# Optimization experiments

Hardware: AMD Instinct MI355X
Metric: run time of the kernel (lower is better)

## Reference

```python
import jax, jax.numpy as jnp
import numpy as np

D_MODEL, N_HEAD, D_HEAD = 192, 16, 6
INNER = N_HEAD * D_HEAD  # 96
LN_EPS = 1e-9
INF = 1e6


def _rel_pos_embeds(S):
    # Funnel get_position_embeds, relative_shift path, block 0
    half = D_MODEL // 2
    freq = jnp.arange(half, dtype=jnp.float32)
    inv_freq = 1.0 / (10000.0 ** (freq / half))
    rel_pos_id = jnp.arange(-2 * S, 2 * S, dtype=jnp.float32)  # [4S]
    sinusoid = rel_pos_id[:, None] * inv_freq[None, :]          # [4S, half]
    pos_embed = jnp.concatenate([jnp.sin(sinusoid), jnp.cos(sinusoid)], axis=-1)  # [4S, D]
    # block 0: relative_pos(pos, stride=1) = arange(S, -S, -1), offset by 2S
    idx = jnp.arange(S, -S, -1) + 2 * S  # [2S]
    return pos_embed[idx]  # [2S, D]


def _relative_shift_gather(pos_attn, context_len):
    # shift = 1 (q_len == context_len)
    B, n, S, M = pos_attn.shape  # M = 2*S
    pa = pos_attn.reshape(B, n, M, S)[:, :, 1:, :]
    pa = pa.reshape(B, n, S, M - 1)[..., :context_len]
    return pa


def setup_inputs() -> dict:
    key = jax.random.key(0)
    ks = jax.random.split(key, 12)
    B, S = 4, 1024
    s = 0.02
    return {
        "x": jax.random.normal(ks[0], (B, S, D_MODEL), dtype=jnp.float32),
        "mask0": jnp.ones((B, S), dtype=jnp.float32),
        "Wq": jax.random.normal(ks[1], (D_MODEL, INNER), dtype=jnp.float32) * s,
        "Wk": jax.random.normal(ks[2], (D_MODEL, INNER), dtype=jnp.float32) * s,
        "bk": jnp.zeros((INNER,), dtype=jnp.float32),
        "Wv": jax.random.normal(ks[3], (D_MODEL, INNER), dtype=jnp.float32) * s,
        "bv": jnp.zeros((INNER,), dtype=jnp.float32),
        "Wo": jax.random.normal(ks[4], (INNER, D_MODEL), dtype=jnp.float32) * s,
        "bo": jnp.zeros((D_MODEL,), dtype=jnp.float32),
        "r_w_bias": jax.random.normal(ks[5], (N_HEAD, D_HEAD), dtype=jnp.float32) * s,
        "r_r_bias": jax.random.normal(ks[6], (N_HEAD, D_HEAD), dtype=jnp.float32) * s,
        "r_kernel": jax.random.normal(ks[7], (D_MODEL, N_HEAD, D_HEAD), dtype=jnp.float32) * s,
        "gamma": jnp.ones((D_MODEL,), dtype=jnp.float32),
        "beta": jnp.zeros((D_MODEL,), dtype=jnp.float32),
    }


def reference(x, mask0, Wq, Wk, bk, Wv, bv, Wo, bo, r_w_bias, r_r_bias, r_kernel, gamma, beta):
    B, S, _ = x.shape
    scale = 1.0 / np.sqrt(D_HEAD).astype(np.float32)

    q = (x @ Wq).reshape(B, S, N_HEAD, D_HEAD) * scale       # q_head pre-scaled
    k = (x @ Wk + bk).reshape(B, S, N_HEAD, D_HEAD)
    v = (x @ Wv + bv).reshape(B, S, N_HEAD, D_HEAD)

    # content score
    content = jnp.einsum("bind,bjnd->bnij", q + r_w_bias * scale, k)

    # positional score with relative shift
    r = _rel_pos_embeds(S)                                    # [2S, D]
    r_head = jnp.einsum("td,dnh->tnh", r, r_kernel)           # [2S, n, h]
    pos_attn = jnp.einsum("binh,tnh->bnit", q + r_r_bias * scale, r_head)  # [B,n,S,2S]
    pos_attn = _relative_shift_gather(pos_attn, S)            # [B,n,S,S]

    attn_score = content + pos_attn  # token_type_attn = 0 (no token_type_ids)
    attn_score = attn_score - INF * (1.0 - mask0[:, None, None, :])
    attn_prob = jax.nn.softmax(attn_score, axis=-1)

    attn_vec = jnp.einsum("bnij,bjnd->bind", attn_prob, v)    # [B,S,n,h]
    attn_out = attn_vec.reshape(B, S, INNER) @ Wo + bo

    h = x + attn_out
    mu = jnp.mean(h, axis=-1, keepdims=True)
    var = jnp.mean(jnp.square(h - mu), axis=-1, keepdims=True)
    out = (h - mu) / jnp.sqrt(var + LN_EPS) * gamma + beta
    return out
```

## Files before the change

### kernel.cpp

```cpp
#include <hip/hip_runtime.h>
#include <hip/hip_bf16.h>
#include <math.h>

#define LOG2E 1.4426950408889634f
#define IS6   0.4082482904638630f

typedef _Float16 h2 __attribute__((ext_vector_type(2)));

#if defined(__has_builtin)
#if __has_builtin(__builtin_amdgcn_fdot2)
#define FDOT2(a,b,c) __builtin_amdgcn_fdot2((a),(b),(c),false)
#endif
#if __has_builtin(__builtin_amdgcn_exp2f)
#define EXP2(x) __builtin_amdgcn_exp2f(x)
#endif
#endif
#ifndef FDOT2
#define FDOT2(a,b,c) ((float)(a).x*(float)(b).x + (float)(a).y*(float)(b).y + (c))
#endif
#ifndef EXP2
#define EXP2(x) exp2f(x)
#endif

__device__ __forceinline__ unsigned packh2(float x, float y) {
    h2 v; v.x = (_Float16)x; v.y = (_Float16)y;
    return *(unsigned*)&v;
}
__device__ __forceinline__ h2 ash2(unsigned u) { return *(h2*)&u; }
__device__ __forceinline__ unsigned ah2(h2 v) { return *(unsigned*)&v; }

#if defined(__has_builtin)
#if __has_builtin(__builtin_amdgcn_cvt_pkrtz)
__device__ __forceinline__ h2 pk2(float a, float b) {
    auto r = __builtin_amdgcn_cvt_pkrtz(a, b);
    union { decltype(r) f; h2 h; } c; c.f = r; return c.h;
}
#define HAVE_PK2 1
#endif
#endif
#ifndef HAVE_PK2
__device__ __forceinline__ h2 pk2(float a, float b) {
    h2 v; v.x = (_Float16)a; v.y = (_Float16)b; return v;
}
#endif

__global__ __launch_bounds__(96)
void k_wpack(const float* __restrict__ Wq, const float* __restrict__ Wk,
             const float* __restrict__ Wv, unsigned* __restrict__ Whp) {
    int bid = blockIdx.x;
    int mat = bid / 96, dp = bid - mat * 96;
    const float* W = mat == 0 ? Wq : (mat == 1 ? Wk : Wv);
    int c = threadIdx.x;
    float w0 = W[(2 * dp) * 96 + c];
    float w1 = W[(2 * dp + 1) * 96 + c];
    Whp[(mat * 96 + c) * 96 + dp] = packh2(w0, w1);
}

__global__ __launch_bounds__(256)
void k_pre(const float* __restrict__ x, const unsigned* __restrict__ Whp,
           const float* __restrict__ bk, const float* __restrict__ bv,
           const float* __restrict__ rwb, const float* __restrict__ rrb,
           const float* __restrict__ rk,
           unsigned* __restrict__ QWt, unsigned* __restrict__ QRt,
           unsigned* __restrict__ Kpl, unsigned* __restrict__ Vpl,
           unsigned short* __restrict__ phiB) {
    __shared__ unsigned xs[64 * 97];
    __shared__ float rrowS[4 * 192];
    int tid = threadIdx.x;
    if (blockIdx.x < 1152) {
        int rt = blockIdx.x / 18, qb = blockIdx.x - rt * 18;
        int row0 = rt * 64;
        for (int idx = tid; idx < 6144; idx += 256) {
            int r = idx / 96, dpp = idx - r * 96;
            float2 xv = *(const float2*)&x[(size_t)(row0 + r) * 192 + dpp * 2];
            xs[r * 97 + dpp] = packh2(xv.x, xv.y);
        }
        __syncthreads();
        int quad = __builtin_amdgcn_readfirstlane(tid >> 6);
        int sl = tid & 63;
        int cq = qb * 4 + quad;
        int c0 = cq * 4;
        int mat = c0 / 96, col0 = c0 - mat * 96;
        const unsigned* wb0 = Whp + (mat * 96 + col0) * 96;
        const unsigned* wb1 = wb0 + 96;
        const unsigned* wb2 = wb0 + 192;
        const unsigned* wb3 = wb0 + 288;
        const unsigned* xr = xs + sl * 97;
        float a0 = 0.f, a1 = 0.f, a2 = 0.f, a3 = 0.f;
        #pragma unroll 8
        for (int dp = 0; dp < 96; ++dp) {
            h2 xp = ash2(xr[dp]);
            a0 = FDOT2(xp, ash2(wb0[dp]), a0);
            a1 = FDOT2(xp, ash2(wb1[dp]), a1);
            a2 = FDOT2(xp, ash2(wb2[dp]), a2);
            a3 = FDOT2(xp, ash2(wb3[dp]), a3);
        }
        float av[4] = {a0, a1, a2, a3};
        int row = row0 + sl, b = row >> 10, s = row & 1023;
        if (mat == 0) {
            #pragma unroll
            for (int pp = 0; pp < 2; ++pp) {
                int cA = col0 + 2 * pp;
                int pg = cA >> 1;
                int nn = pg / 3, hp = pg - nn * 3;
                int bnn = b * 16 + nn;
                unsigned qw = packh2((av[2*pp]   + rwb[cA])   * (IS6 * LOG2E),
                                     (av[2*pp+1] + rwb[cA+1]) * (IS6 * LOG2E));
                unsigned qr = packh2((av[2*pp]   + rrb[cA])   * (IS6 * LOG2E),
                                     (av[2*pp+1] + rrb[cA+1]) * (IS6 * LOG2E));
                size_t qo = ((size_t)(hp * 64 + bnn) << 10) + s;
                QWt[qo] = qw;
                QRt[qo] = qr;
            }
        } else if (mat == 1) {
            #pragma unroll
            for (int pp = 0; pp < 2; ++pp) {
                int cA = col0 + 2 * pp;
                int pg = cA >> 1;
                int nn = pg / 3, hp = pg - nn * 3;
                int bnn = b * 16 + nn;
                Kpl[((size_t)(hp * 64 + bnn) << 10) + s] =
                    packh2(av[2*pp] + bk[cA], av[2*pp+1] + bk[cA+1]);
            }
        } else {
            #pragma unroll
            for (int pp = 0; pp < 2; ++pp) {
                int cA = col0 + 2 * pp;
                int pg = cA >> 1;
                int nn = pg / 3, hp = pg - nn * 3;
                int bnn = b * 16 + nn;
                Vpl[((size_t)(hp * 64 + bnn) << 10) + s] =
                    packh2(av[2*pp] + bv[cA], av[2*pp+1] + bv[cA+1]);
            }
        }
    } else {
        int t0 = (blockIdx.x - 1152) * 4;
        for (int idx = tid; idx < 768; idx += 256) {
            int tl = idx / 192, d = idx - tl * 192;
            int dd = d < 96 ? d : d - 96;
            float w = exp2f(-(float)dd * 0.13841367062030676f);
            float ang = (float)(1024 - (t0 + tl)) * w;
            rrowS[idx] = (d < 96) ? __sinf(ang) : __cosf(ang);
        }
        __syncthreads();
        if (tid < 192) {
            int c = tid % 96, tg = tid / 96;
            float acc0 = 0.f, acc1 = 0.f;
            #pragma unroll 4
            for (int d = 0; d < 192; ++d) {
                float wv = rk[d * 96 + c];
                acc0 += rrowS[(tg * 2 + 0) * 192 + d] * wv;
                acc1 += rrowS[(tg * 2 + 1) * 192 + d] * wv;
            }
            int n = c / 6, h = c - n * 6;
            _Float16 v0 = (_Float16)acc0, v1 = (_Float16)acc1;
            phiB[(n * 2048 + t0 + tg * 2 + 0) * 8 + h] = *(unsigned short*)&v0;
            phiB[(n * 2048 + t0 + tg * 2 + 1) * 8 + h] = *(unsigned short*)&v1;
            if (tg == 0 && c < 32) {
                int nn = c >> 1, hh = 6 + (c & 1);
                #pragma unroll
                for (int k = 0; k < 4; ++k)
                    phiB[(nn * 2048 + t0 + k) * 8 + hh] = 0;
            }
        }
    }
}

#define SWZ(r) ((r) ^ (((r) >> 3) & 7))
__global__ __launch_bounds__(256, 6)
void k_attn(const unsigned* __restrict__ QWt, const unsigned* __restrict__ QRt,
            const unsigned* __restrict__ Kpl, const unsigned* __restrict__ Vpl,
            const float* __restrict__ mask0,
            const unsigned short* __restrict__ phiB,
            uint4* __restrict__ P) {
    __shared__ uint4 phiS[1088];
    __shared__ uint4 kS[64];
    __shared__ unsigned vS[192];
    int tid = threadIdx.x;
    int jc = blockIdx.x, n = blockIdx.y, b = blockIdx.z;
    int j0 = jc * 64;
    int bn = b * 16 + n;

    const uint4* phg = (const uint4*)phiB + (n * 2048 + j0 + 1);
    for (int r = tid; r < 1088; r += 256) phiS[SWZ(r)] = phg[r];
    if (tid < 64) {
        int j = j0 + tid;
        size_t base = ((size_t)bn << 10) + j;
        float mt = 1e6f * (mask0[b * 1024 + j] - 1.0f) * LOG2E;
        kS[tid] = make_uint4(Kpl[base], Kpl[base + 65536], Kpl[base + 131072],
                             __float_as_uint(mt));
    } else if (tid < 128) {
        int r = tid - 64;
        int j = j0 + r;
        size_t base = ((size_t)bn << 10) + j;
        vS[r * 3 + 0] = Vpl[base];
        vS[r * 3 + 1] = Vpl[base + 65536];
        vS[r * 3 + 2] = Vpl[base + 131072];
    }
    __syncthreads();

    int iA = tid * 4;
    h2 qw[4][3], qr[4][3];
    #pragma unroll
    for (int hp = 0; hp < 3; ++hp) {
        size_t off = (size_t)hp * 65536 + ((size_t)bn << 10) + iA;
        uint4 qa = *(const uint4*)&QWt[off];
        qw[0][hp] = ash2(qa.x); qw[1][hp] = ash2(qa.y);
        qw[2][hp] = ash2(qa.z); qw[3][hp] = ash2(qa.w);
        uint4 ra = *(const uint4*)&QRt[off];
        qr[0][hp] = ash2(ra.x); qr[1][hp] = ash2(ra.y);
        qr[2][hp] = ash2(ra.z); qr[3][hp] = ash2(ra.w);
    }

    float den[4] = {0.f, 0.f, 0.f, 0.f};
    h2 zero2; zero2.x = (_Float16)0.f; zero2.y = (_Float16)0.f;
    h2 ac0[4], ac1[4], ac2[4];
    #pragma unroll
    for (int q = 0; q < 4; ++q) { ac0[q] = zero2; ac1[q] = zero2; ac2[q] = zero2; }

    int Cb = 1023 - iA;
    uint4 ph[4];
    ph[3] = phiS[SWZ(Cb - 1)];
    ph[2] = phiS[SWZ(Cb - 2)];
    ph[1] = phiS[SWZ(Cb - 3)];
    uint4 nxt = phiS[SWZ(Cb)];

    #pragma unroll 4
    for (int jj = 0; jj < 64; ++jj) {
        uint4 K = kS[jj];
        unsigned Vx = vS[3 * jj], Vy = vS[3 * jj + 1], Vz = vS[3 * jj + 2];
        ph[jj & 3] = nxt;
        nxt = phiS[SWZ(Cb + jj + 1)];
        float mt = __uint_as_float(K.w);
        h2 v01 = ash2(Vx), v23 = ash2(Vy), v45 = ash2(Vz);
        #pragma unroll
        for (int q = 0; q < 4; ++q) {
            uint4 p = ph[(jj - q) & 3];
            float sc = FDOT2(ash2(K.x), qw[q][0],
                       FDOT2(ash2(K.y), qw[q][1],
                       FDOT2(ash2(K.z), qw[q][2], mt)));
            sc = FDOT2(ash2(p.x), qr[q][0],
                 FDOT2(ash2(p.y), qr[q][1],
                 FDOT2(ash2(p.z), qr[q][2], sc)));
            float e = EXP2(sc);
            den[q] += e;
            h2 e2 = pk2(e, e);
            ac0[q] += e2 * v01;
            ac1[q] += e2 * v23;
            ac2[q] += e2 * v45;
        }
    }
    size_t pb = ((size_t)(jc * 64 + bn)) << 10;
    #pragma unroll
    for (int q = 0; q < 4; ++q) {
        uint4 st;
        st.x = __float_as_uint(den[q]);
        st.y = ah2(ac0[q]); st.z = ah2(ac1[q]); st.w = ah2(ac2[q]);
        P[pb + q * 256 + tid] = st;
    }
}

__global__ __launch_bounds__(256)
void k_comb(const uint4* __restrict__ P, float* __restrict__ AV) {
    int flat = blockIdx.x * 256 + threadIdx.x;
    int bn = flat >> 10, rem = flat & 1023;
    int q = rem >> 8, tt = rem & 255;
    int i = tt * 4 + q;
    int b = bn >> 4, n = bn & 15;
    float d = 0.f, s0 = 0.f, s1 = 0.f, s2 = 0.f, s3 = 0.f, s4 = 0.f, s5 = 0.f;
    #pragma unroll
    for (int jc = 0; jc < 16; ++jc) {
        uint4 u = P[(((size_t)(jc * 64 + bn)) << 10) + rem];
        h2 x0 = ash2(u.y), x1 = ash2(u.z), x2 = ash2(u.w);
        d  += __uint_as_float(u.x);
        s0 += (float)x0.x; s1 += (float)x0.y;
        s2 += (float)x1.x; s3 += (float)x1.y;
        s4 += (float)x2.x; s5 += (float)x2.y;
    }
    float inv = 1.0f / d;
    float* o = AV + ((size_t)(b * 1024 + i)) * 96 + n * 6;
    o[0] = s0 * inv; o[1] = s1 * inv; o[2] = s2 * inv;
    o[3] = s3 * inv; o[4] = s4 * inv; o[5] = s5 * inv;
}

__global__ __launch_bounds__(256)
void k_out(const float* __restrict__ AV, const float* __restrict__ Wo,
           const float* __restrict__ bo, const float* __restrict__ x,
           const float* __restrict__ gamma, const float* __restrict__ beta,
           float* __restrict__ out) {
    __shared__ unsigned WoS[96 * 96];
    __shared__ float avS[8 * 96];
    int tid = threadIdx.x;
    int row0 = blockIdx.x * 8;
    for (int idx = tid; idx < 9216; idx += 256) {
        int c = idx / 96, pd = idx - c * 96;
        float2 w = *(const float2*)&Wo[c * 192 + pd * 2];
        WoS[idx] = packh2(w.x, w.y);
    }
    for (int idx = tid; idx < 768; idx += 256)
        avS[idx] = AV[(size_t)row0 * 96 + idx];
    __syncthreads();

    int lane = tid & 63, wv = tid >> 6;
    bool act = lane < 48;
    int d0 = lane * 4;
    #pragma unroll
    for (int rr = 0; rr < 2; ++rr) {
        int r = wv * 2 + rr, row = row0 + r;
        float ax = 0.f, ay = 0.f, az = 0.f, aw = 0.f;
        if (act) {
            float4 bq = *(const float4*)&bo[d0];
            float4 xq = *(const float4*)&x[(size_t)row * 192 + d0];
            ax = bq.x + xq.x; ay = bq.y + xq.y; az = bq.z + xq.z; aw = bq.w + xq.w;
            for (int c2 = 0; c2 < 96; ++c2) {
                float a = avS[r * 96 + c2];
                uint2 wp = *(uint2*)&WoS[c2 * 96 + lane * 2];
                h2 w0 = ash2(wp.x), w1 = ash2(wp.y);
                ax += a * (float)w0.x; ay += a * (float)w0.y;
                az += a * (float)w1.x; aw += a * (float)w1.y;
            }
        }
        float sum = act ? (ax + ay + az + aw) : 0.f;
        #pragma unroll
        for (int off = 32; off; off >>= 1) sum += __shfl_xor(sum, off, 64);
        float mu = sum * (1.0f / 192.0f);
        float dx = ax - mu, dy = ay - mu, dz = az - mu, dw = aw - mu;
        float vs = act ? (dx * dx + dy * dy + dz * dz + dw * dw) : 0.f;
        #pragma unroll
        for (int off = 32; off; off >>= 1) vs += __shfl_xor(vs, off, 64);
        float rstd = rsqrtf(vs * (1.0f / 192.0f) + 1e-9f);
        if (act) {
            float4 g = *(const float4*)&gamma[d0];
            float4 bb = *(const float4*)&beta[d0];
            float4 rv;
            rv.x = dx * rstd * g.x + bb.x;
            rv.y = dy * rstd * g.y + bb.y;
            rv.z = dz * rstd * g.z + bb.z;
            rv.w = dw * rstd * g.w + bb.w;
            *(float4*)&out[(size_t)row * 192 + d0] = rv;
        }
    }
}

extern "C" void kernel_launch(void* const* d_in, const int* in_sizes, int n_in,
                              void* d_out, int out_size, void* d_ws, size_t ws_size,
                              hipStream_t stream) {
    const float* x        = (const float*)d_in[0];
    const float* mask0    = (const float*)d_in[1];
    const float* Wq       = (const float*)d_in[2];
    const float* Wk       = (const float*)d_in[3];
    const float* bk       = (const float*)d_in[4];
    const float* Wv       = (const float*)d_in[5];
    const float* bv       = (const float*)d_in[6];
    const float* Wo       = (const float*)d_in[7];
    const float* bo       = (const float*)d_in[8];
    const float* rwb      = (const float*)d_in[9];
    const float* rrb      = (const float*)d_in[10];
    const float* r_kernel = (const float*)d_in[11];
    const float* gamma    = (const float*)d_in[12];
    const float* beta     = (const float*)d_in[13];
    float* out = (float*)d_out;

    unsigned* QWt = (unsigned*)d_ws;
    unsigned* QRt = QWt + 196608;
    unsigned* Kpl = QRt + 196608;
    unsigned* Vpl = Kpl + 196608;
    uint4*    P   = (uint4*)(Vpl + 196608);
    unsigned short* phiB = (unsigned short*)(P + 1048576);
    unsigned* Whp = (unsigned*)(phiB + 262144);
    float*    AV  = (float*)(Whp + 27648);

    k_wpack<<<288, 96, 0, stream>>>(Wq, Wk, Wv, Whp);
    k_pre<<<1664, 256, 0, stream>>>(x, Whp, bk, bv, rwb, rrb, r_kernel,
                                    QWt, QRt, Kpl, Vpl, phiB);
    k_attn<<<dim3(16, 16, 4), 256, 0, stream>>>(QWt, QRt, Kpl, Vpl, mask0, phiB, P);
    k_comb<<<256, 256, 0, stream>>>(P, AV);
    k_out<<<512, 256, 0, stream>>>(AV, Wo, bo, x, gamma, beta, out);
}
```

Before: 91.25 us.

## Interleave packed QKV weights as uint4, stage in LDS, reorder pre blocks

```diff
diff --git a/kernel.cpp b/kernel.cpp
--- a/kernel.cpp
+++ b/kernel.cpp
@@ -46,18 +46,23 @@
 
 __global__ __launch_bounds__(96)
 void k_wpack(const float* __restrict__ Wq, const float* __restrict__ Wk,
-             const float* __restrict__ Wv, unsigned* __restrict__ Whp) {
-    int bid = blockIdx.x;
-    int mat = bid / 96, dp = bid - mat * 96;
+             const float* __restrict__ Wv, uint4* __restrict__ Whp4) {
+    int cq = blockIdx.x;
+    int dp = threadIdx.x;
+    int mat = cq / 24, c0 = (cq - mat * 24) * 4;
     const float* W = mat == 0 ? Wq : (mat == 1 ? Wk : Wv);
-    int c = threadIdx.x;
-    float w0 = W[(2 * dp) * 96 + c];
-    float w1 = W[(2 * dp + 1) * 96 + c];
-    Whp[(mat * 96 + c) * 96 + dp] = packh2(w0, w1);
+    float4 r0 = *(const float4*)&W[(2 * dp) * 96 + c0];
+    float4 r1 = *(const float4*)&W[(2 * dp + 1) * 96 + c0];
+    uint4 v;
+    v.x = packh2(r0.x, r1.x);
+    v.y = packh2(r0.y, r1.y);
+    v.z = packh2(r0.z, r1.z);
+    v.w = packh2(r0.w, r1.w);
+    Whp4[cq * 96 + dp] = v;
 }
 
 __global__ __launch_bounds__(256)
-void k_pre(const float* __restrict__ x, const unsigned* __restrict__ Whp,
+void k_pre(const float* __restrict__ x, const uint4* __restrict__ Whp4,
            const float* __restrict__ bk, const float* __restrict__ bv,
            const float* __restrict__ rwb, const float* __restrict__ rrb,
            const float* __restrict__ rk,
@@ -65,35 +70,67 @@
            unsigned* __restrict__ Kpl, unsigned* __restrict__ Vpl,
            unsigned short* __restrict__ phiB) {
     __shared__ unsigned xs[64 * 97];
+    __shared__ uint4 Wlds[384];
     __shared__ float rrowS[4 * 192];
     int tid = threadIdx.x;
-    if (blockIdx.x < 1152) {
-        int rt = blockIdx.x / 18, qb = blockIdx.x - rt * 18;
+    if (blockIdx.x < 512) {
+        int t0 = blockIdx.x * 4;
+        for (int idx = tid; idx < 768; idx += 256) {
+            int tl = idx / 192, d = idx - tl * 192;
+            int dd = d < 96 ? d : d - 96;
+            float w = exp2f(-(float)dd * 0.13841367062030676f);
+            float ang = (float)(1024 - (t0 + tl)) * w;
+            rrowS[idx] = (d < 96) ? __sinf(ang) : __cosf(ang);
+        }
+        __syncthreads();
+        if (tid < 192) {
+            int c = tid % 96, tg = tid / 96;
+            float acc0 = 0.f, acc1 = 0.f;
+            #pragma unroll 4
+            for (int d = 0; d < 192; ++d) {
+                float wv = rk[d * 96 + c];
+                acc0 += rrowS[(tg * 2 + 0) * 192 + d] * wv;
+                acc1 += rrowS[(tg * 2 + 1) * 192 + d] * wv;
+            }
+            int n = c / 6, h = c - n * 6;
+            _Float16 v0 = (_Float16)acc0, v1 = (_Float16)acc1;
+            phiB[(n * 2048 + t0 + tg * 2 + 0) * 8 + h] = *(unsigned short*)&v0;
+            phiB[(n * 2048 + t0 + tg * 2 + 1) * 8 + h] = *(unsigned short*)&v1;
+            if (tg == 0 && c < 32) {
+                int nn = c >> 1, hh = 6 + (c & 1);
+                #pragma unroll
+                for (int k = 0; k < 4; ++k)
+                    phiB[(nn * 2048 + t0 + k) * 8 + hh] = 0;
+            }
+        }
+    } else {
+        int qkvb = blockIdx.x - 512;
+        int rt = qkvb / 18, qb = qkvb - rt * 18;
         int row0 = rt * 64;
         for (int idx = tid; idx < 6144; idx += 256) {
             int r = idx / 96, dpp = idx - r * 96;
             float2 xv = *(const float2*)&x[(size_t)(row0 + r) * 192 + dpp * 2];
             xs[r * 97 + dpp] = packh2(xv.x, xv.y);
         }
+        for (int idx = tid; idx < 384; idx += 256)
+            Wlds[idx] = Whp4[qb * 384 + idx];
         __syncthreads();
-        int quad = __builtin_amdgcn_readfirstlane(tid >> 6);
+        int quad = tid >> 6;
         int sl = tid & 63;
         int cq = qb * 4 + quad;
-        int c0 = cq * 4;
-        int mat = c0 / 96, col0 = c0 - mat * 96;
-        const unsigned* wb0 = Whp + (mat * 96 + col0) * 96;
-        const unsigned* wb1 = wb0 + 96;
-        const unsigned* wb2 = wb0 + 192;
-        const unsigned* wb3 = wb0 + 288;
+        int c0g = cq * 4;
+        int mat = c0g / 96, col0 = c0g - mat * 96;
+        const uint4* wq4 = &Wlds[quad * 96];
         const unsigned* xr = xs + sl * 97;
         float a0 = 0.f, a1 = 0.f, a2 = 0.f, a3 = 0.f;
         #pragma unroll 8
         for (int dp = 0; dp < 96; ++dp) {
+            uint4 w4 = wq4[dp];
             h2 xp = ash2(xr[dp]);
-            a0 = FDOT2(xp, ash2(wb0[dp]), a0);
-            a1 = FDOT2(xp, ash2(wb1[dp]), a1);
-            a2 = FDOT2(xp, ash2(wb2[dp]), a2);
-            a3 = FDOT2(xp, ash2(wb3[dp]), a3);
+            a0 = FDOT2(xp, ash2(w4.x), a0);
+            a1 = FDOT2(xp, ash2(w4.y), a1);
+            a2 = FDOT2(xp, ash2(w4.z), a2);
+            a3 = FDOT2(xp, ash2(w4.w), a3);
         }
         float av[4] = {a0, a1, a2, a3};
         int row = row0 + sl, b = row >> 10, s = row & 1023;
@@ -133,36 +170,6 @@
                     packh2(av[2*pp] + bv[cA], av[2*pp+1] + bv[cA+1]);
             }
         }
-    } else {
-        int t0 = (blockIdx.x - 1152) * 4;
-        for (int idx = tid; idx < 768; idx += 256) {
-            int tl = idx / 192, d = idx - tl * 192;
-            int dd = d < 96 ? d : d - 96;
-            float w = exp2f(-(float)dd * 0.13841367062030676f);
-            float ang = (float)(1024 - (t0 + tl)) * w;
-            rrowS[idx] = (d < 96) ? __sinf(ang) : __cosf(ang);
-        }
-        __syncthreads();
-        if (tid < 192) {
-            int c = tid % 96, tg = tid / 96;
-            float acc0 = 0.f, acc1 = 0.f;
-            #pragma unroll 4
-            for (int d = 0; d < 192; ++d) {
-                float wv = rk[d * 96 + c];
-                acc0 += rrowS[(tg * 2 + 0) * 192 + d] * wv;
-                acc1 += rrowS[(tg * 2 + 1) * 192 + d] * wv;
-            }
-            int n = c / 6, h = c - n * 6;
-            _Float16 v0 = (_Float16)acc0, v1 = (_Float16)acc1;
-            phiB[(n * 2048 + t0 + tg * 2 + 0) * 8 + h] = *(unsigned short*)&v0;
-            phiB[(n * 2048 + t0 + tg * 2 + 1) * 8 + h] = *(unsigned short*)&v1;
-            if (tg == 0 && c < 32) {
-                int nn = c >> 1, hh = 6 + (c & 1);
-                #pragma unroll
-                for (int k = 0; k < 4; ++k)
-                    phiB[(nn * 2048 + t0 + k) * 8 + hh] = 0;
-            }
-        }
     }
 }
 
@@ -175,7 +182,7 @@
             uint4* __restrict__ P) {
     __shared__ uint4 phiS[1088];
     __shared__ uint4 kS[64];
-    __shared__ unsigned vS[192];
+    __shared__ uint4 vS[64];
     int tid = threadIdx.x;
     int jc = blockIdx.x, n = blockIdx.y, b = blockIdx.z;
     int j0 = jc * 64;
@@ -193,9 +200,7 @@
         int r = tid - 64;
         int j = j0 + r;
         size_t base = ((size_t)bn << 10) + j;
-        vS[r * 3 + 0] = Vpl[base];
-        vS[r * 3 + 1] = Vpl[base + 65536];
-        vS[r * 3 + 2] = Vpl[base + 131072];
+        vS[r] = make_uint4(Vpl[base], Vpl[base + 65536], Vpl[base + 131072], 0u);
     }
     __syncthreads();
 
@@ -228,11 +233,11 @@
     #pragma unroll 4
     for (int jj = 0; jj < 64; ++jj) {
         uint4 K = kS[jj];
-        unsigned Vx = vS[3 * jj], Vy = vS[3 * jj + 1], Vz = vS[3 * jj + 2];
+        uint4 V = vS[jj];
         ph[jj & 3] = nxt;
         nxt = phiS[SWZ(Cb + jj + 1)];
         float mt = __uint_as_float(K.w);
-        h2 v01 = ash2(Vx), v23 = ash2(Vy), v45 = ash2(Vz);
+        h2 v01 = ash2(V.x), v23 = ash2(V.y), v45 = ash2(V.z);
         #pragma unroll
         for (int q = 0; q < 4; ++q) {
             uint4 p = ph[(jj - q) & 3];
@@ -367,11 +372,11 @@
     unsigned* Vpl = Kpl + 196608;
     uint4*    P   = (uint4*)(Vpl + 196608);
     unsigned short* phiB = (unsigned short*)(P + 1048576);
-    unsigned* Whp = (unsigned*)(phiB + 262144);
-    float*    AV  = (float*)(Whp + 27648);
-
-    k_wpack<<<288, 96, 0, stream>>>(Wq, Wk, Wv, Whp);
-    k_pre<<<1664, 256, 0, stream>>>(x, Whp, bk, bv, rwb, rrb, r_kernel,
+    uint4*    Whp4 = (uint4*)(phiB + 262144);
+    float*    AV  = (float*)(Whp4 + 6912);
+
+    k_wpack<<<72, 96, 0, stream>>>(Wq, Wk, Wv, Whp4);
+    k_pre<<<1664, 256, 0, stream>>>(x, Whp4, bk, bv, rwb, rrb, r_kernel,
                                     QWt, QRt, Kpl, Vpl, phiB);
     k_attn<<<dim3(16, 16, 4), 256, 0, stream>>>(QWt, QRt, Kpl, Vpl, mask0, phiB, P);
     k_comb<<<256, 256, 0, stream>>>(P, AV);
```

Result: slower. 98.01 us (+7.4%).
